# Kernel optimization log

Hardware: AMD Instinct MI355X
Metric: run time of the kernel (lower is better)

Reference implementation:

```python
import jax, jax.numpy as jnp
import numpy as np

B, N, IN, H, D = 4096, 65536, 64, 512, 256  # samples, total neighbors, input_size, hidden_size, dist_dim
EMB_IN = IN + H + D  # 832, social_emb Linear input dim


def setup_inputs() -> dict:
    key = jax.random.key(0)
    ks = jax.random.split(key, 12)
    # contiguous ragged segments tiling [0, N): random sorted boundaries
    boundaries = jnp.sort(jax.random.randint(ks[0], (B - 1,), 0, N, dtype=jnp.int32))
    starts = jnp.concatenate([jnp.zeros((1,), jnp.int32), boundaries])
    ends = jnp.concatenate([boundaries, jnp.full((1,), N, jnp.int32)])
    s = 0.02
    return {
        "traj_input": jax.random.normal(ks[1], (B, H), jnp.float32),
        "neighbor_t": jax.random.normal(ks[2], (N, IN), jnp.float32),
        "dist": jax.random.normal(ks[3], (N, D), jnp.float32),
        "ht": jax.random.normal(ks[4], (N, H), jnp.float32),
        "W_emb": jax.random.normal(ks[5], (EMB_IN, H), jnp.float32) * s,
        "b_emb": jnp.zeros((H,), jnp.float32),
        "w_ih": jax.random.normal(ks[6], (3 * H, H), jnp.float32) * s,
        "w_hh": jax.random.normal(ks[7], (3 * H, H), jnp.float32) * s,
        "b_ih": jnp.zeros((3 * H,), jnp.float32),
        "b_hh": jnp.zeros((3 * H,), jnp.float32),
        "neighbors_idx_start": starts,
        "neighbors_idx_end": ends,
    }


def reference(traj_input, neighbor_t, dist, ht, W_emb, b_emb, w_ih, w_hh, b_ih, b_hh,
              neighbors_idx_start, neighbors_idx_end):
    Nn = neighbor_t.shape[0]
    # map each flat neighbor row to its owning sample (segments are contiguous & sorted)
    sample_id = jnp.searchsorted(neighbors_idx_start, jnp.arange(Nn, dtype=neighbors_idx_start.dtype), side='right') - 1
    # ragged gather + concat: [N, IN + H + D]
    x = jnp.concatenate([neighbor_t, traj_input[sample_id], dist], axis=-1)
    emb = jax.nn.relu(x @ W_emb + b_emb)  # social_emb: Linear + ReLU
    # PyTorch GRUCell math
    gi = emb @ w_ih.T + b_ih  # [N, 3H]
    gh = ht @ w_hh.T + b_hh   # [N, 3H]
    i_r, i_z, i_n = jnp.split(gi, 3, axis=-1)
    h_r, h_z, h_n = jnp.split(gh, 3, axis=-1)
    r = jax.nn.sigmoid(i_r + h_r)
    z = jax.nn.sigmoid(i_z + h_z)
    n = jnp.tanh(i_n + r * h_n)
    return (1.0 - z) * n + z * ht  # [N, H], concat of per-sample GRU outputs
```

## Files before the change

### kernel.cpp

```cpp
#include <hip/hip_runtime.h>
#include <stdint.h>

#define BSAMP 4096
#define NTOT  65536
#define INW   64
#define HW    512
#define DW    256
#define EMB_IN 832

typedef unsigned short ushort_t;
using bf16x8 = __attribute__((ext_vector_type(8))) short;
using f32x4  = __attribute__((ext_vector_type(4))) float;

__device__ __forceinline__ ushort_t f2bf(float f) {
    unsigned int x = __builtin_bit_cast(unsigned int, f);
    x = x + 0x7fff + ((x >> 16) & 1);
    return (ushort_t)(x >> 16);
}

__device__ __forceinline__ void async16(const void* g, void* l) {
    __builtin_amdgcn_global_load_lds((const __attribute__((address_space(1))) unsigned int*)g,
                                     (__attribute__((address_space(3))) unsigned int*)l,
                                     16, 0, 0);
}

__global__ __launch_bounds__(256) void k_cvt4(const float* __restrict__ in,
                                              ushort_t* __restrict__ out, int n4) {
    int i = blockIdx.x * 256 + threadIdx.x;
    if (i >= n4) return;
    float4 v = *(const float4*)(in + (size_t)i * 4);
    uint2 o;
    o.x = (unsigned)f2bf(v.x) | ((unsigned)f2bf(v.y) << 16);
    o.y = (unsigned)f2bf(v.z) | ((unsigned)f2bf(v.w) << 16);
    *(uint2*)(out + (size_t)i * 4) = o;
}

__global__ __launch_bounds__(256) void k_transpose(const float* __restrict__ in,
                                                   ushort_t* __restrict__ out) {
    int i = blockIdx.x * 256 + threadIdx.x;
    if (i >= HW * EMB_IN) return;
    int n = i / EMB_IN;
    int k = i - n * EMB_IN;
    out[i] = f2bf(in[k * HW + n]);
}

__global__ __launch_bounds__(256) void k_build_wrz(const float* __restrict__ wih,
                                                   const float* __restrict__ whh,
                                                   ushort_t* __restrict__ wrz) {
    int i = blockIdx.x * 256 + threadIdx.x;
    int row = i >> 10, k = i & 1023;
    float v = (k < 512) ? wih[row * 512 + k] : whh[row * 512 + (k - 512)];
    wrz[i] = f2bf(v);
}

__global__ __launch_bounds__(256) void k_build_wnn(const float* __restrict__ wih,
                                                   const float* __restrict__ whh,
                                                   ushort_t* __restrict__ wnn) {
    int i = blockIdx.x * 256 + threadIdx.x;
    int h = i >> 10, k = i & 1023;
    float v = (k < 512) ? wih[(1024 + h) * 512 + k] : whh[(1024 + h) * 512 + (k - 512)];
    wnn[i] = f2bf(v);
}

__global__ __launch_bounds__(256) void k_sid(const int* __restrict__ starts,
                                             int* __restrict__ sid) {
    int n = blockIdx.x * 256 + threadIdx.x;
    int lo = 0, hi = BSAMP - 1;
    #pragma unroll
    for (int it = 0; it < 12; ++it) {
        int mid = (lo + hi + 1) >> 1;
        if (starts[mid] <= n) lo = mid; else hi = mid - 1;
    }
    sid[n] = lo;
}

__global__ __launch_bounds__(256) void k_cvt_ht(const float* __restrict__ ht,
                                                ushort_t* __restrict__ Acat, int n128) {
    int i = blockIdx.x * 256 + threadIdx.x;
    if (i >= n128) return;
    int row = i >> 7, c4 = i & 127;
    float4 v = *(const float4*)(ht + row * 512 + c4 * 4);
    ushort_t* d = Acat + (size_t)row * 1024 + 512 + c4 * 4;
    d[0] = f2bf(v.x); d[1] = f2bf(v.y); d[2] = f2bf(v.z); d[3] = f2bf(v.w);
}

__global__ __launch_bounds__(256, 2) void k_emb(const ushort_t* __restrict__ neighbf,
                                                const ushort_t* __restrict__ trajbf,
                                                const ushort_t* __restrict__ distbf,
                                                const ushort_t* __restrict__ wembT,
                                                const float* __restrict__ bemb,
                                                const int* __restrict__ sid,
                                                ushort_t* __restrict__ Acat,
                                                int base) {
    __shared__ short As[2][128 * 64];
    __shared__ short Bs[2][128 * 64];

    const int tid = threadIdx.x;
    const int b = blockIdx.x;
    const int total = gridDim.x;
    const int lg = (b & 7) * (total >> 3) + (b >> 3);
    const int cb = lg & 3, rb = lg >> 2;
    const int lrow0 = rb * 128;
    const int row0g = base + lrow0;
    const int wave = tid >> 6, lane = tid & 63;
    const int wm = wave & 1, wn = wave >> 1;
    const int quad = lane >> 4, l15 = lane & 15;
    const int mb = wm * 64, nb = wn * 64;
    const int srow = lane >> 3, sc8 = lane & 7;
    const int swz = (l15 & 7) << 3;

    f32x4 acc[4][4];
    #pragma unroll
    for (int i = 0; i < 4; ++i)
        #pragma unroll
        for (int j = 0; j < 4; ++j) acc[i][j] = (f32x4){0.f, 0.f, 0.f, 0.f};

    auto stage = [&](int kk, int buf) {
        #pragma unroll
        for (int p = 0; p < 4; ++p) {
            int row = p * 32 + wave * 8 + srow;
            async16(wembT + (cb * 128 + row) * EMB_IN + kk * 64 + (sc8 ^ srow) * 8,
                    &Bs[buf][p * 2048 + wave * 512]);
        }
        #pragma unroll
        for (int p = 0; p < 4; ++p) {
            int row = p * 32 + wave * 8 + srow;
            const ushort_t* src;
            if (kk == 0)
                src = neighbf + (size_t)(row0g + row) * 64 + (sc8 ^ srow) * 8;
            else if (kk <= 8)
                src = trajbf + (size_t)sid[row0g + row] * HW + (kk - 1) * 64 + (sc8 ^ srow) * 8;
            else
                src = distbf + (size_t)(row0g + row) * 256 + (kk - 9) * 64 + (sc8 ^ srow) * 8;
            async16(src, &As[buf][p * 2048 + wave * 512]);
        }
    };

    auto compute = [&](int buf) {
        __builtin_amdgcn_s_setprio(1);
        #pragma unroll
        for (int ks = 0; ks < 2; ++ks) {
            const int kb = (ks * 32 + quad * 8) ^ swz;
            bf16x8 af[4], bfr[4];
            #pragma unroll
            for (int i = 0; i < 4; ++i)
                af[i] = *(const bf16x8*)(&As[buf][(mb + i * 16 + l15) * 64 + kb]);
            #pragma unroll
            for (int j = 0; j < 4; ++j)
                bfr[j] = *(const bf16x8*)(&Bs[buf][(nb + j * 16 + l15) * 64 + kb]);
            #pragma unroll
            for (int i = 0; i < 4; ++i)
                #pragma unroll
                for (int j = 0; j < 4; ++j)
                    acc[i][j] = __builtin_amdgcn_mfma_f32_16x16x32_bf16(af[i], bfr[j], acc[i][j], 0, 0, 0);
        }
        __builtin_amdgcn_s_setprio(0);
    };

    stage(0, 0);
    __syncthreads();
    for (int kk = 0; kk < 13; ++kk) {
        int buf = kk & 1;
        if (kk < 12) stage(kk + 1, buf ^ 1);
        compute(buf);
        __syncthreads();
    }

    #pragma unroll
    for (int j = 0; j < 4; ++j) {
        int gn = cb * 128 + nb + j * 16 + l15;
        float bias = bemb[gn];
        #pragma unroll
        for (int i = 0; i < 4; ++i) {
            int lm0 = lrow0 + mb + i * 16 + quad * 4;
            #pragma unroll
            for (int r = 0; r < 4; ++r) {
                float v = acc[i][j][r] + bias;
                v = v > 0.f ? v : 0.f;
                Acat[(size_t)(lm0 + r) * 1024 + gn] = f2bf(v);
            }
        }
    }
}

__global__ __launch_bounds__(256, 2) void k_gru(const ushort_t* __restrict__ Acat,
                                                const float* __restrict__ ht,
                                                const ushort_t* __restrict__ wrz,
                                                const ushort_t* __restrict__ wnn,
                                                const float* __restrict__ bih,
                                                const float* __restrict__ bhh,
                                                float* __restrict__ out,
                                                int base) {
    __shared__ short As[2][128 * 64];
    __shared__ short Bs[2][3 * 64 * 64];

    const int tid = threadIdx.x;
    const int b = blockIdx.x;
    const int total = gridDim.x;
    const int lg = (b & 7) * (total >> 3) + (b >> 3);
    const int hb = lg & 7, rb = lg >> 3;
    const int lrow0 = rb * 128;
    const int row0g = base + lrow0;
    const int h0 = hb * 64;
    const int wave = tid >> 6, lane = tid & 63;
    const int wm = wave & 1, wn = wave >> 1;
    const int quad = lane >> 4, l15 = lane & 15;
    const int mb = wm * 64, nb = wn * 32;
    const int srow = lane >> 3, sc8 = lane & 7;
    const int swz = (l15 & 7) << 3;

    f32x4 accR[4][2], accZ[4][2], accNI[4][2], accNH[4][2];
    #pragma unroll
    for (int i = 0; i < 4; ++i)
        #pragma unroll
        for (int j = 0; j < 2; ++j) {
            accR[i][j] = (f32x4){0.f, 0.f, 0.f, 0.f};
            accZ[i][j] = (f32x4){0.f, 0.f, 0.f, 0.f};
            accNI[i][j] = (f32x4){0.f, 0.f, 0.f, 0.f};
            accNH[i][j] = (f32x4){0.f, 0.f, 0.f, 0.f};
        }

    const ushort_t* Wr = wrz + (size_t)h0 * 1024;
    const ushort_t* Wz = wrz + (size_t)(512 + h0) * 1024;
    const ushort_t* Wn = wnn + (size_t)h0 * 1024;

    auto stage = [&](int kk, int buf) {
        #pragma unroll
        for (int p = 0; p < 4; ++p) {
            int row = p * 32 + wave * 8 + srow;
            async16(Acat + (size_t)(lrow0 + row) * 1024 + kk * 64 + (sc8 ^ srow) * 8,
                    &As[buf][p * 2048 + wave * 512]);
        }
        #pragma unroll
        for (int p = 0; p < 2; ++p) {
            int row = p * 32 + wave * 8 + srow;
            int goff = row * 1024 + kk * 64 + (sc8 ^ srow) * 8;
            int loff = p * 2048 + wave * 512;
            async16(Wr + goff, &Bs[buf][loff]);
            async16(Wz + goff, &Bs[buf][4096 + loff]);
            async16(Wn + goff, &Bs[buf][8192 + loff]);
        }
    };

    auto compute = [&](int buf, f32x4 (&accN)[4][2]) {
        __builtin_amdgcn_s_setprio(1);
        #pragma unroll
        for (int ks = 0; ks < 2; ++ks) {
            const int kb = (ks * 32 + quad * 8) ^ swz;
            bf16x8 af[4];
            #pragma unroll
            for (int i = 0; i < 4; ++i)
                af[i] = *(const bf16x8*)(&As[buf][(mb + i * 16 + l15) * 64 + kb]);

            bf16x8 br0 = *(const bf16x8*)(&Bs[buf][(nb + l15) * 64 + kb]);
            bf16x8 br1 = *(const bf16x8*)(&Bs[buf][(nb + 16 + l15) * 64 + kb]);
            #pragma unroll
            for (int i = 0; i < 4; ++i) {
                accR[i][0] = __builtin_amdgcn_mfma_f32_16x16x32_bf16(af[i], br0, accR[i][0], 0, 0, 0);
                accR[i][1] = __builtin_amdgcn_mfma_f32_16x16x32_bf16(af[i], br1, accR[i][1], 0, 0, 0);
            }
            bf16x8 bz0 = *(const bf16x8*)(&Bs[buf][4096 + (nb + l15) * 64 + kb]);
            bf16x8 bz1 = *(const bf16x8*)(&Bs[buf][4096 + (nb + 16 + l15) * 64 + kb]);
            #pragma unroll
            for (int i = 0; i < 4; ++i) {
                accZ[i][0] = __builtin_amdgcn_mfma_f32_16x16x32_bf16(af[i], bz0, accZ[i][0], 0, 0, 0);
                accZ[i][1] = __builtin_amdgcn_mfma_f32_16x16x32_bf16(af[i], bz1, accZ[i][1], 0, 0, 0);
            }
            bf16x8 bn0 = *(const bf16x8*)(&Bs[buf][8192 + (nb + l15) * 64 + kb]);
            bf16x8 bn1 = *(const bf16x8*)(&Bs[buf][8192 + (nb + 16 + l15) * 64 + kb]);
            #pragma unroll
            for (int i = 0; i < 4; ++i) {
                accN[i][0] = __builtin_amdgcn_mfma_f32_16x16x32_bf16(af[i], bn0, accN[i][0], 0, 0, 0);
                accN[i][1] = __builtin_amdgcn_mfma_f32_16x16x32_bf16(af[i], bn1, accN[i][1], 0, 0, 0);
            }
        }
        __builtin_amdgcn_s_setprio(0);
    };

    stage(0, 0);
    __syncthreads();
    for (int kk = 0; kk < 8; ++kk) {
        int buf = kk & 1;
        stage(kk + 1, buf ^ 1);
        compute(buf, accNI);
        __syncthreads();
    }
    for (int kk = 8; kk < 16; ++kk) {
        int buf = kk & 1;
        if (kk < 15) stage(kk + 1, buf ^ 1);
        compute(buf, accNH);
        __syncthreads();
    }

    #pragma unroll
    for (int j = 0; j < 2; ++j) {
        int gn = h0 + nb + j * 16 + l15;
        float br = bih[gn] + bhh[gn];
        float bz = bih[gn + 512] + bhh[gn + 512];
        float bin = bih[gn + 1024], bhn = bhh[gn + 1024];
        #pragma unroll
        for (int i = 0; i < 4; ++i) {
            int gm0 = row0g + mb + i * 16 + quad * 4;
            #pragma unroll
            for (int r = 0; r < 4; ++r) {
                int gm = gm0 + r;
                float rg = 1.f / (1.f + __expf(-(accR[i][j][r] + br)));
                float zg = 1.f / (1.f + __expf(-(accZ[i][j][r] + bz)));
                float ng = tanhf(accNI[i][j][r] + bin + rg * (accNH[i][j][r] + bhn));
                float hp = ht[(size_t)gm * HW + gn];
                out[(size_t)gm * HW + gn] = (1.f - zg) * ng + zg * hp;
            }
        }
    }
}

extern "C" void kernel_launch(void* const* d_in, const int* in_sizes, int n_in,
                              void* d_out, int out_size, void* d_ws, size_t ws_size,
                              hipStream_t stream) {
    const float* traj   = (const float*)d_in[0];
    const float* neigh  = (const float*)d_in[1];
    const float* dist   = (const float*)d_in[2];
    const float* ht     = (const float*)d_in[3];
    const float* W_emb  = (const float*)d_in[4];
    const float* b_emb  = (const float*)d_in[5];
    const float* w_ih   = (const float*)d_in[6];
    const float* w_hh   = (const float*)d_in[7];
    const float* b_ih   = (const float*)d_in[8];
    const float* b_hh   = (const float*)d_in[9];
    const int*   starts = (const int*)d_in[10];

    char* ws = (char*)d_ws;
    int*      sid     = (int*)ws;
    ushort_t* wembT   = (ushort_t*)(ws + 262144);
    ushort_t* wrz     = (ushort_t*)(ws + 1114112);
    ushort_t* wnn     = (ushort_t*)(ws + 3211264);
    ushort_t* trajbf  = (ushort_t*)(ws + 4259840);
    ushort_t* neighbf = (ushort_t*)(ws + 8454144);
    ushort_t* distbf  = (ushort_t*)(ws + 16842752);
    ushort_t* Acat    = (ushort_t*)(ws + 50397184);

    float* out = (float*)d_out;

    long long avail = (long long)ws_size - 50397184LL;
    int chunk_rows = (int)(avail / 2048);
    chunk_rows &= ~255;
    if (chunk_rows > NTOT) chunk_rows = NTOT;
    if (chunk_rows < 256) chunk_rows = 256;

    k_sid<<<dim3(NTOT / 256), dim3(256), 0, stream>>>(starts, sid);
    k_cvt4<<<dim3(BSAMP * HW / 1024), dim3(256), 0, stream>>>(traj, trajbf, BSAMP * HW / 4);
    k_cvt4<<<dim3(NTOT * INW / 1024), dim3(256), 0, stream>>>(neigh, neighbf, NTOT * INW / 4);
    k_cvt4<<<dim3(NTOT * DW / 1024), dim3(256), 0, stream>>>(dist, distbf, NTOT * DW / 4);
    k_transpose<<<dim3((HW * EMB_IN + 255) / 256), dim3(256), 0, stream>>>(W_emb, wembT);
    k_build_wrz<<<dim3(1024 * 1024 / 256), dim3(256), 0, stream>>>(w_ih, w_hh, wrz);
    k_build_wnn<<<dim3(512 * 1024 / 256), dim3(256), 0, stream>>>(w_ih, w_hh, wnn);

    for (int base = 0; base < NTOT; base += chunk_rows) {
        int rows = NTOT - base;
        if (rows > chunk_rows) rows = chunk_rows;
        int n128 = rows * 128;
        k_cvt_ht<<<dim3((n128 + 255) / 256), dim3(256), 0, stream>>>(ht + (size_t)base * HW, Acat, n128);
        k_emb<<<dim3(4 * (rows / 128)), dim3(256), 0, stream>>>(neighbf, trajbf, distbf, wembT,
                                                                b_emb, sid, Acat, base);
        k_gru<<<dim3(8 * (rows / 128)), dim3(256), 0, stream>>>(Acat, ht, wrz, wnn,
                                                                b_ih, b_hh, out, base);
    }
}
```

Baseline: 729.5 us.

## Load weight fragments directly from global and triple-buffer activation tiles in LDS

In both the embedding GEMM and the GRU GEMM, the weight (B) operand is no longer staged in LDS. Each lane now reads its bf16x8 fragments straight from global memory into registers, relying on cache for reuse. The activation (A) tiles move to a three-buffer LDS ring that uses one barrier per k-step and explicit vmcnt waits in place of two __syncthreads. This is meant to cut LDS traffic, LDS footprint and barrier cost. The risk is that the in-order vmcnt counter makes waits on the direct B loads also wait on the A prefetch, and that the per-lane global weight reads are poorly coalesced and add latency.

```diff
diff --git a/kernel.cpp b/kernel.cpp
--- a/kernel.cpp
+++ b/kernel.cpp
@@ -92,8 +92,7 @@
                                                 const int* __restrict__ sid,
                                                 ushort_t* __restrict__ Acat,
                                                 int base) {
-    __shared__ short As[2][128 * 64];
-    __shared__ short Bs[2][128 * 64];
+    __shared__ short As[3][128 * 64];
 
     const int tid = threadIdx.x;
     const int b = blockIdx.x;
@@ -115,39 +114,46 @@
         #pragma unroll
         for (int j = 0; j < 4; ++j) acc[i][j] = (f32x4){0.f, 0.f, 0.f, 0.f};
 
-    auto stage = [&](int kk, int buf) {
+    const ushort_t* nptr[4];
+    const ushort_t* tptr[4];
+    const ushort_t* dptr[4];
+    #pragma unroll
+    for (int p = 0; p < 4; ++p) {
+        int row = p * 32 + wave * 8 + srow;
+        int sw8 = (sc8 ^ srow) * 8;
+        nptr[p] = neighbf + (size_t)(row0g + row) * 64 + sw8;
+        tptr[p] = trajbf + (size_t)sid[row0g + row] * HW + sw8;
+        dptr[p] = distbf + (size_t)(row0g + row) * 256 + sw8;
+    }
+    const ushort_t* bptr[4];
+    #pragma unroll
+    for (int j = 0; j < 4; ++j)
+        bptr[j] = wembT + (size_t)(cb * 128 + nb + j * 16 + l15) * EMB_IN + quad * 8;
+
+    auto stageA = [&](int kk, int buf) {
         #pragma unroll
         for (int p = 0; p < 4; ++p) {
-            int row = p * 32 + wave * 8 + srow;
-            async16(wembT + (cb * 128 + row) * EMB_IN + kk * 64 + (sc8 ^ srow) * 8,
-                    &Bs[buf][p * 2048 + wave * 512]);
-        }
-        #pragma unroll
-        for (int p = 0; p < 4; ++p) {
-            int row = p * 32 + wave * 8 + srow;
             const ushort_t* src;
-            if (kk == 0)
-                src = neighbf + (size_t)(row0g + row) * 64 + (sc8 ^ srow) * 8;
-            else if (kk <= 8)
-                src = trajbf + (size_t)sid[row0g + row] * HW + (kk - 1) * 64 + (sc8 ^ srow) * 8;
-            else
-                src = distbf + (size_t)(row0g + row) * 256 + (kk - 9) * 64 + (sc8 ^ srow) * 8;
+            if (kk == 0)       src = nptr[p];
+            else if (kk <= 8)  src = tptr[p] + (kk - 1) * 64;
+            else               src = dptr[p] + (kk - 9) * 64;
             async16(src, &As[buf][p * 2048 + wave * 512]);
         }
     };
 
-    auto compute = [&](int buf) {
+    auto compute = [&](int kk, int buf) {
         __builtin_amdgcn_s_setprio(1);
         #pragma unroll
         for (int ks = 0; ks < 2; ++ks) {
             const int kb = (ks * 32 + quad * 8) ^ swz;
+            const int kg = kk * 64 + ks * 32;
             bf16x8 af[4], bfr[4];
             #pragma unroll
             for (int i = 0; i < 4; ++i)
                 af[i] = *(const bf16x8*)(&As[buf][(mb + i * 16 + l15) * 64 + kb]);
             #pragma unroll
             for (int j = 0; j < 4; ++j)
-                bfr[j] = *(const bf16x8*)(&Bs[buf][(nb + j * 16 + l15) * 64 + kb]);
+                bfr[j] = *(const bf16x8*)(bptr[j] + kg);
             #pragma unroll
             for (int i = 0; i < 4; ++i)
                 #pragma unroll
@@ -157,13 +163,19 @@
         __builtin_amdgcn_s_setprio(0);
     };
 
-    stage(0, 0);
-    __syncthreads();
+    stageA(0, 0);
+    int buf = 0;
     for (int kk = 0; kk < 13; ++kk) {
-        int buf = kk & 1;
-        if (kk < 12) stage(kk + 1, buf ^ 1);
-        compute(buf);
-        __syncthreads();
+        int nbuf = buf + 1; if (nbuf == 3) nbuf = 0;
+        if (kk < 12) {
+            stageA(kk + 1, nbuf);
+            asm volatile("s_waitcnt vmcnt(4)" ::: "memory");
+        } else {
+            asm volatile("s_waitcnt vmcnt(0)" ::: "memory");
+        }
+        __builtin_amdgcn_s_barrier();
+        compute(kk, buf);
+        buf = nbuf;
     }
 
     #pragma unroll
@@ -191,8 +203,7 @@
                                                 const float* __restrict__ bhh,
                                                 float* __restrict__ out,
                                                 int base) {
-    __shared__ short As[2][128 * 64];
-    __shared__ short Bs[2][3 * 64 * 64];
+    __shared__ short As[3][128 * 64];
 
     const int tid = threadIdx.x;
     const int b = blockIdx.x;
@@ -220,54 +231,55 @@
             accNH[i][j] = (f32x4){0.f, 0.f, 0.f, 0.f};
         }
 
+    const ushort_t* aptr[4];
+    #pragma unroll
+    for (int p = 0; p < 4; ++p) {
+        int row = p * 32 + wave * 8 + srow;
+        aptr[p] = Acat + (size_t)(lrow0 + row) * 1024 + (sc8 ^ srow) * 8;
+    }
     const ushort_t* Wr = wrz + (size_t)h0 * 1024;
     const ushort_t* Wz = wrz + (size_t)(512 + h0) * 1024;
     const ushort_t* Wn = wnn + (size_t)h0 * 1024;
-
-    auto stage = [&](int kk, int buf) {
-        #pragma unroll
-        for (int p = 0; p < 4; ++p) {
-            int row = p * 32 + wave * 8 + srow;
-            async16(Acat + (size_t)(lrow0 + row) * 1024 + kk * 64 + (sc8 ^ srow) * 8,
-                    &As[buf][p * 2048 + wave * 512]);
-        }
-        #pragma unroll
-        for (int p = 0; p < 2; ++p) {
-            int row = p * 32 + wave * 8 + srow;
-            int goff = row * 1024 + kk * 64 + (sc8 ^ srow) * 8;
-            int loff = p * 2048 + wave * 512;
-            async16(Wr + goff, &Bs[buf][loff]);
-            async16(Wz + goff, &Bs[buf][4096 + loff]);
-            async16(Wn + goff, &Bs[buf][8192 + loff]);
-        }
+    const ushort_t* br_p0 = Wr + (size_t)(nb + l15) * 1024 + quad * 8;
+    const ushort_t* br_p1 = Wr + (size_t)(nb + 16 + l15) * 1024 + quad * 8;
+    const ushort_t* bz_p0 = Wz + (size_t)(nb + l15) * 1024 + quad * 8;
+    const ushort_t* bz_p1 = Wz + (size_t)(nb + 16 + l15) * 1024 + quad * 8;
+    const ushort_t* bn_p0 = Wn + (size_t)(nb + l15) * 1024 + quad * 8;
+    const ushort_t* bn_p1 = Wn + (size_t)(nb + 16 + l15) * 1024 + quad * 8;
+
+    auto stageA = [&](int kk, int buf) {
+        #pragma unroll
+        for (int p = 0; p < 4; ++p)
+            async16(aptr[p] + kk * 64, &As[buf][p * 2048 + wave * 512]);
     };
 
-    auto compute = [&](int buf, f32x4 (&accN)[4][2]) {
+    auto compute = [&](int kk, int buf, f32x4 (&accN)[4][2]) {
         __builtin_amdgcn_s_setprio(1);
         #pragma unroll
         for (int ks = 0; ks < 2; ++ks) {
             const int kb = (ks * 32 + quad * 8) ^ swz;
+            const int kg = kk * 64 + ks * 32;
             bf16x8 af[4];
             #pragma unroll
             for (int i = 0; i < 4; ++i)
                 af[i] = *(const bf16x8*)(&As[buf][(mb + i * 16 + l15) * 64 + kb]);
 
-            bf16x8 br0 = *(const bf16x8*)(&Bs[buf][(nb + l15) * 64 + kb]);
-            bf16x8 br1 = *(const bf16x8*)(&Bs[buf][(nb + 16 + l15) * 64 + kb]);
+            bf16x8 br0 = *(const bf16x8*)(br_p0 + kg);
+            bf16x8 br1 = *(const bf16x8*)(br_p1 + kg);
             #pragma unroll
             for (int i = 0; i < 4; ++i) {
                 accR[i][0] = __builtin_amdgcn_mfma_f32_16x16x32_bf16(af[i], br0, accR[i][0], 0, 0, 0);
                 accR[i][1] = __builtin_amdgcn_mfma_f32_16x16x32_bf16(af[i], br1, accR[i][1], 0, 0, 0);
             }
-            bf16x8 bz0 = *(const bf16x8*)(&Bs[buf][4096 + (nb + l15) * 64 + kb]);
-            bf16x8 bz1 = *(const bf16x8*)(&Bs[buf][4096 + (nb + 16 + l15) * 64 + kb]);
+            bf16x8 bz0 = *(const bf16x8*)(bz_p0 + kg);
+            bf16x8 bz1 = *(const bf16x8*)(bz_p1 + kg);
             #pragma unroll
             for (int i = 0; i < 4; ++i) {
                 accZ[i][0] = __builtin_amdgcn_mfma_f32_16x16x32_bf16(af[i], bz0, accZ[i][0], 0, 0, 0);
                 accZ[i][1] = __builtin_amdgcn_mfma_f32_16x16x32_bf16(af[i], bz1, accZ[i][1], 0, 0, 0);
             }
-            bf16x8 bn0 = *(const bf16x8*)(&Bs[buf][8192 + (nb + l15) * 64 + kb]);
-            bf16x8 bn1 = *(const bf16x8*)(&Bs[buf][8192 + (nb + 16 + l15) * 64 + kb]);
+            bf16x8 bn0 = *(const bf16x8*)(bn_p0 + kg);
+            bf16x8 bn1 = *(const bf16x8*)(bn_p1 + kg);
             #pragma unroll
             for (int i = 0; i < 4; ++i) {
                 accN[i][0] = __builtin_amdgcn_mfma_f32_16x16x32_bf16(af[i], bn0, accN[i][0], 0, 0, 0);
@@ -277,19 +289,20 @@
         __builtin_amdgcn_s_setprio(0);
     };
 
-    stage(0, 0);
-    __syncthreads();
-    for (int kk = 0; kk < 8; ++kk) {
-        int buf = kk & 1;
-        stage(kk + 1, buf ^ 1);
-        compute(buf, accNI);
-        __syncthreads();
-    }
-    for (int kk = 8; kk < 16; ++kk) {
-        int buf = kk & 1;
-        if (kk < 15) stage(kk + 1, buf ^ 1);
-        compute(buf, accNH);
-        __syncthreads();
+    stageA(0, 0);
+    int buf = 0;
+    for (int kk = 0; kk < 16; ++kk) {
+        int nbuf = buf + 1; if (nbuf == 3) nbuf = 0;
+        if (kk < 15) {
+            stageA(kk + 1, nbuf);
+            asm volatile("s_waitcnt vmcnt(4)" ::: "memory");
+        } else {
+            asm volatile("s_waitcnt vmcnt(0)" ::: "memory");
+        }
+        __builtin_amdgcn_s_barrier();
+        if (kk < 8) compute(kk, buf, accNI);
+        else        compute(kk, buf, accNH);
+        buf = nbuf;
     }
 
     #pragma unroll
```

Result: slower. 1.654 ms (+126.7%).

## Fuse fp32-to-bf16 conversion of neighbor, dist and ht into GEMM staging

Applied to the files above, without the earlier changes.

Removes the separate bf16 conversion kernels for neighbor_t, dist and ht. The GEMM kernels now load fp32 tiles directly, convert them in registers and write them swizzled into LDS. Acat shrinks to hold only the embedding half, with rows of 512. This cuts an extra global write/read pass and several launches. In exchange those k-steps lose the async global-to-LDS path and use synchronous loads inside the pipeline, which can stall the double-buffered overlap.

```diff
diff --git a/kernel.cpp b/kernel.cpp
--- a/kernel.cpp
+++ b/kernel.cpp
@@ -74,19 +74,9 @@
     sid[n] = lo;
 }
 
-__global__ __launch_bounds__(256) void k_cvt_ht(const float* __restrict__ ht,
-                                                ushort_t* __restrict__ Acat, int n128) {
-    int i = blockIdx.x * 256 + threadIdx.x;
-    if (i >= n128) return;
-    int row = i >> 7, c4 = i & 127;
-    float4 v = *(const float4*)(ht + row * 512 + c4 * 4);
-    ushort_t* d = Acat + (size_t)row * 1024 + 512 + c4 * 4;
-    d[0] = f2bf(v.x); d[1] = f2bf(v.y); d[2] = f2bf(v.z); d[3] = f2bf(v.w);
-}
-
-__global__ __launch_bounds__(256, 2) void k_emb(const ushort_t* __restrict__ neighbf,
+__global__ __launch_bounds__(256, 2) void k_emb(const float* __restrict__ neigh,
                                                 const ushort_t* __restrict__ trajbf,
-                                                const ushort_t* __restrict__ distbf,
+                                                const float* __restrict__ dist,
                                                 const ushort_t* __restrict__ wembT,
                                                 const float* __restrict__ bemb,
                                                 const int* __restrict__ sid,
@@ -122,17 +112,26 @@
             async16(wembT + (cb * 128 + row) * EMB_IN + kk * 64 + (sc8 ^ srow) * 8,
                     &Bs[buf][p * 2048 + wave * 512]);
         }
-        #pragma unroll
-        for (int p = 0; p < 4; ++p) {
-            int row = p * 32 + wave * 8 + srow;
-            const ushort_t* src;
-            if (kk == 0)
-                src = neighbf + (size_t)(row0g + row) * 64 + (sc8 ^ srow) * 8;
-            else if (kk <= 8)
-                src = trajbf + (size_t)sid[row0g + row] * HW + (kk - 1) * 64 + (sc8 ^ srow) * 8;
-            else
-                src = distbf + (size_t)(row0g + row) * 256 + (kk - 9) * 64 + (sc8 ^ srow) * 8;
-            async16(src, &As[buf][p * 2048 + wave * 512]);
+        if (kk >= 1 && kk <= 8) {
+            #pragma unroll
+            for (int p = 0; p < 4; ++p) {
+                int row = p * 32 + wave * 8 + srow;
+                async16(trajbf + (size_t)sid[row0g + row] * HW + (kk - 1) * 64 + (sc8 ^ srow) * 8,
+                        &As[buf][p * 2048 + wave * 512]);
+            }
+        } else {
+            const float* srcb;
+            int rs;
+            if (kk == 0) { srcb = neigh + (size_t)row0g * INW;                  rs = INW; }
+            else         { srcb = dist + (size_t)row0g * DW + (kk - 9) * 64;    rs = DW;  }
+            #pragma unroll
+            for (int p = 0; p < 8; ++p) {
+                int idx = p * 256 + tid;
+                int row = idx >> 4, c4 = idx & 15;
+                float4 v = *(const float4*)(srcb + (size_t)row * rs + c4 * 4);
+                ushort_t* d = (ushort_t*)&As[buf][row * 64 + ((c4 * 4) ^ ((row & 7) << 3))];
+                d[0] = f2bf(v.x); d[1] = f2bf(v.y); d[2] = f2bf(v.z); d[3] = f2bf(v.w);
+            }
         }
     };
 
@@ -177,7 +176,7 @@
             for (int r = 0; r < 4; ++r) {
                 float v = acc[i][j][r] + bias;
                 v = v > 0.f ? v : 0.f;
-                Acat[(size_t)(lm0 + r) * 1024 + gn] = f2bf(v);
+                Acat[(size_t)(lm0 + r) * 512 + gn] = f2bf(v);
             }
         }
     }
@@ -225,11 +224,23 @@
     const ushort_t* Wn = wnn + (size_t)h0 * 1024;
 
     auto stage = [&](int kk, int buf) {
-        #pragma unroll
-        for (int p = 0; p < 4; ++p) {
-            int row = p * 32 + wave * 8 + srow;
-            async16(Acat + (size_t)(lrow0 + row) * 1024 + kk * 64 + (sc8 ^ srow) * 8,
-                    &As[buf][p * 2048 + wave * 512]);
+        if (kk < 8) {
+            #pragma unroll
+            for (int p = 0; p < 4; ++p) {
+                int row = p * 32 + wave * 8 + srow;
+                async16(Acat + (size_t)(lrow0 + row) * 512 + kk * 64 + (sc8 ^ srow) * 8,
+                        &As[buf][p * 2048 + wave * 512]);
+            }
+        } else {
+            const float* srcb = ht + (size_t)row0g * HW + (kk - 8) * 64;
+            #pragma unroll
+            for (int p = 0; p < 8; ++p) {
+                int idx = p * 256 + tid;
+                int row = idx >> 4, c4 = idx & 15;
+                float4 v = *(const float4*)(srcb + (size_t)row * HW + c4 * 4);
+                ushort_t* d = (ushort_t*)&As[buf][row * 64 + ((c4 * 4) ^ ((row & 7) << 3))];
+                d[0] = f2bf(v.x); d[1] = f2bf(v.y); d[2] = f2bf(v.z); d[3] = f2bf(v.w);
+            }
         }
         #pragma unroll
         for (int p = 0; p < 2; ++p) {
@@ -335,22 +346,18 @@
     ushort_t* wrz     = (ushort_t*)(ws + 1114112);
     ushort_t* wnn     = (ushort_t*)(ws + 3211264);
     ushort_t* trajbf  = (ushort_t*)(ws + 4259840);
-    ushort_t* neighbf = (ushort_t*)(ws + 8454144);
-    ushort_t* distbf  = (ushort_t*)(ws + 16842752);
-    ushort_t* Acat    = (ushort_t*)(ws + 50397184);
+    ushort_t* Acat    = (ushort_t*)(ws + 8454144);
 
     float* out = (float*)d_out;
 
-    long long avail = (long long)ws_size - 50397184LL;
-    int chunk_rows = (int)(avail / 2048);
+    long long avail = (long long)ws_size - 8454144LL;
+    int chunk_rows = (int)(avail / 1024);
     chunk_rows &= ~255;
     if (chunk_rows > NTOT) chunk_rows = NTOT;
     if (chunk_rows < 256) chunk_rows = 256;
 
     k_sid<<<dim3(NTOT / 256), dim3(256), 0, stream>>>(starts, sid);
     k_cvt4<<<dim3(BSAMP * HW / 1024), dim3(256), 0, stream>>>(traj, trajbf, BSAMP * HW / 4);
-    k_cvt4<<<dim3(NTOT * INW / 1024), dim3(256), 0, stream>>>(neigh, neighbf, NTOT * INW / 4);
-    k_cvt4<<<dim3(NTOT * DW / 1024), dim3(256), 0, stream>>>(dist, distbf, NTOT * DW / 4);
     k_transpose<<<dim3((HW * EMB_IN + 255) / 256), dim3(256), 0, stream>>>(W_emb, wembT);
     k_build_wrz<<<dim3(1024 * 1024 / 256), dim3(256), 0, stream>>>(w_ih, w_hh, wrz);
     k_build_wnn<<<dim3(512 * 1024 / 256), dim3(256), 0, stream>>>(w_ih, w_hh, wnn);
@@ -358,9 +365,7 @@
     for (int base = 0; base < NTOT; base += chunk_rows) {
         int rows = NTOT - base;
         if (rows > chunk_rows) rows = chunk_rows;
-        int n128 = rows * 128;
-        k_cvt_ht<<<dim3((n128 + 255) / 256), dim3(256), 0, stream>>>(ht + (size_t)base * HW, Acat, n128);
-        k_emb<<<dim3(4 * (rows / 128)), dim3(256), 0, stream>>>(neighbf, trajbf, distbf, wembT,
+        k_emb<<<dim3(4 * (rows / 128)), dim3(256), 0, stream>>>(neigh, trajbf, dist, wembT,
                                                                 b_emb, sid, Acat, base);
         k_gru<<<dim3(8 * (rows / 128)), dim3(256), 0, stream>>>(Acat, ht, wrz, wnn,
                                                                 b_ih, b_hh, out, base);
```

Measured after the change: 692.1 us. 5.1% less time.
